# Kernel tuning notes

Measured on AMD Instinct MI355X. Metric: run time of the kernel, lower is better.

Reference implementation:

```python
import jax, jax.numpy as jnp
import numpy as np

NUM_EXPERTS = 8
TOP_K = 2
HIDDEN = 512
INTER = 2048
BALANCE_COEF = 0.01


def setup_inputs() -> dict:
    key = jax.random.key(0)
    ks = jax.random.split(key, 5)
    B, S = 2, 1024
    scale_in = 1.0 / np.sqrt(HIDDEN)
    scale_mid = 1.0 / np.sqrt(INTER)
    return {
        "hidden_states": jax.random.normal(ks[0], (B, S, HIDDEN), jnp.float32),
        "w_router": jax.random.normal(ks[1], (HIDDEN, NUM_EXPERTS), jnp.float32) * scale_in,
        "b_router": jnp.zeros((NUM_EXPERTS,), jnp.float32),
        "w1": jax.random.normal(ks[2], (NUM_EXPERTS, HIDDEN, INTER), jnp.float32) * scale_in,
        "b1": jnp.zeros((NUM_EXPERTS, INTER), jnp.float32),
        "w2": jax.random.normal(ks[3], (NUM_EXPERTS, INTER, HIDDEN), jnp.float32) * scale_mid,
        "b2": jnp.zeros((NUM_EXPERTS, HIDDEN), jnp.float32),
    }


def reference(hidden_states, w_router, b_router, w1, b1, w2, b2):
    B, S, H = hidden_states.shape
    E, K = NUM_EXPERTS, TOP_K

    # ---- Router: softmax over experts, top-k selection, renormalized weights ----
    logits = jnp.einsum("bsh,he->bse", hidden_states, w_router) + b_router  # (B,S,E)
    probs = jax.nn.softmax(logits, axis=-1)
    top_vals, top_idx = jax.lax.top_k(probs, K)                              # (B,S,K)
    routing_weights = top_vals / jnp.sum(top_vals, axis=-1, keepdims=True)   # renorm to sum 1

    # ---- Load-balancing auxiliary loss: coef * E * sum_e f_e * P_e ----
    assign = jax.nn.one_hot(top_idx, E, dtype=probs.dtype)                   # (B,S,K,E)
    f = jnp.mean(assign, axis=(0, 1, 2))                                     # fraction routed per expert
    P = jnp.mean(probs, axis=(0, 1))                                         # mean router prob per expert
    balance_loss = BALANCE_COEF * E * jnp.sum(f * P)

    # ---- Phase 1: flatten (B,S,H) -> (B*S*K, H) token-slots ----
    T = B * S * K
    tokens_flat = jnp.broadcast_to(hidden_states[:, :, None, :], (B, S, K, H)).reshape(T, H)
    weights_flat = routing_weights.reshape(T)
    experts_flat = top_idx.reshape(T)

    # ---- Phase 2: per-expert MLP, masked combine ----
    out_flat = jnp.zeros_like(tokens_flat)
    for e in range(E):
        hmid = jax.nn.gelu(tokens_flat @ w1[e] + b1[e])                      # (T, INTER)
        y = hmid @ w2[e] + b2[e]                                             # (T, H)
        mask = (experts_flat == e)
        out_flat = out_flat + jnp.where(mask[:, None], y * weights_flat[:, None], 0.0)

    # ---- Phase 3: combine over K and residual ----
    combined = out_flat.reshape(B, S, K, H).sum(axis=2)
    output = combined + hidden_states
    return output, balance_loss
```

## Files before the change

### kernel.cpp

```cpp
#include <hip/hip_runtime.h>
#include <math.h>

#define NT 2048
#define TSLOTS 4096
#define HID 512
#define INTER 2048
#define NE 8
#define TM 128
#define BK 32
#define MAXTILES 40

#define WS_HMID      0
#define WS_PROBS     0
#define WS_TOPIDX    65536
#define WS_TOPW      81920
#define WS_TILE_E    20971520
#define WS_TILE_B    20971776
#define WS_TILE_V    20972032
#define WS_PERM      20972288
#define WS_PW        20992768
#define WS_XB        21013248
#define WS_WT        23110400

typedef __attribute__((ext_vector_type(8))) short bf16x8;
typedef __attribute__((ext_vector_type(4))) float f32x4;
typedef __attribute__((ext_vector_type(8))) unsigned short ushort8;

__device__ __forceinline__ unsigned short f2bf(float f) {
    union { float f; unsigned u; } v; v.f = f;
    unsigned r = v.u + 0x7FFF + ((v.u >> 16) & 1);
    return (unsigned short)(r >> 16);
}

__device__ __forceinline__ void gload16(const void* g, void* l) {
    __builtin_amdgcn_global_load_lds(
        (const __attribute__((address_space(1))) unsigned int*)g,
        (__attribute__((address_space(3))) unsigned int*)l, 16, 0, 0);
}

__device__ __forceinline__ float gelu_tanh(float x) {
    float x3 = x * x * x;
    return 0.5f * x * (1.0f + tanhf(0.7978845608028654f * (x + 0.044715f * x3)));
}

__global__ __launch_bounds__(64) void route_k(
    const float* __restrict__ hs, const float* __restrict__ wr,
    const float* __restrict__ br,
    unsigned short* __restrict__ xb, float* __restrict__ out,
    float* __restrict__ probs, int* __restrict__ topidx, float* __restrict__ topw)
{
    int t = blockIdx.x;
    int lane = threadIdx.x;
    const float* x = hs + (size_t)t * HID + lane * 8;
    float4 v0 = *(const float4*)x;
    float4 v1 = *(const float4*)(x + 4);

    float* o = out + (size_t)t * HID + lane * 8;
    *(float4*)o = v0;
    *(float4*)(o + 4) = v1;

    ushort8 ob;
    ob[0] = f2bf(v0.x); ob[1] = f2bf(v0.y); ob[2] = f2bf(v0.z); ob[3] = f2bf(v0.w);
    ob[4] = f2bf(v1.x); ob[5] = f2bf(v1.y); ob[6] = f2bf(v1.z); ob[7] = f2bf(v1.w);
    *(ushort8*)(xb + (size_t)t * HID + lane * 8) = ob;

    float xv[8] = {v0.x, v0.y, v0.z, v0.w, v1.x, v1.y, v1.z, v1.w};
    float acc[NE];
#pragma unroll
    for (int e = 0; e < NE; e++) acc[e] = 0.0f;
    const float* w = wr + (size_t)lane * 8 * NE;
#pragma unroll
    for (int j = 0; j < 8; j++) {
        float4 wa = *(const float4*)(w + j * NE);
        float4 wb = *(const float4*)(w + j * NE + 4);
        acc[0] += xv[j] * wa.x; acc[1] += xv[j] * wa.y;
        acc[2] += xv[j] * wa.z; acc[3] += xv[j] * wa.w;
        acc[4] += xv[j] * wb.x; acc[5] += xv[j] * wb.y;
        acc[6] += xv[j] * wb.z; acc[7] += xv[j] * wb.w;
    }
#pragma unroll
    for (int off = 32; off > 0; off >>= 1) {
#pragma unroll
        for (int e = 0; e < NE; e++) acc[e] += __shfl_down(acc[e], off);
    }
    if (lane == 0) {
        float l[NE], p[NE];
        float m = -1e30f;
#pragma unroll
        for (int e = 0; e < NE; e++) { l[e] = acc[e] + br[e]; m = fmaxf(m, l[e]); }
        float s = 0.0f;
#pragma unroll
        for (int e = 0; e < NE; e++) { p[e] = expf(l[e] - m); s += p[e]; }
        float inv = 1.0f / s;
#pragma unroll
        for (int e = 0; e < NE; e++) { p[e] *= inv; probs[(size_t)t * NE + e] = p[e]; }
        int i1 = 0;
#pragma unroll
        for (int e = 1; e < NE; e++) if (p[e] > p[i1]) i1 = e;
        int i2 = (i1 == 0) ? 1 : 0;
#pragma unroll
        for (int e = 0; e < NE; e++) if (e != i1 && p[e] > p[i2]) i2 = e;
        float denom = 1.0f / (p[i1] + p[i2]);
        topidx[2 * t]     = i1;
        topidx[2 * t + 1] = i2;
        topw[2 * t]       = p[i1] * denom;
        topw[2 * t + 1]   = p[i2] * denom;
    }
}

__global__ __launch_bounds__(256) void plan_k(
    const float* __restrict__ probs, const int* __restrict__ topidx,
    const float* __restrict__ topw,
    int* __restrict__ tile_e, int* __restrict__ tile_b, int* __restrict__ tile_v,
    int* __restrict__ perm, float* __restrict__ pw, float* __restrict__ loss_out)
{
    int tid = threadIdx.x;
    int lane = tid & 63, wave = tid >> 6;

    float ps[NE];
    int c[NE];
#pragma unroll
    for (int e = 0; e < NE; e++) { ps[e] = 0.0f; c[e] = 0; }
    for (int t = tid; t < NT; t += 256) {
        float4 p0 = *(const float4*)&probs[(size_t)t * NE];
        float4 p1 = *(const float4*)&probs[(size_t)t * NE + 4];
        ps[0] += p0.x; ps[1] += p0.y; ps[2] += p0.z; ps[3] += p0.w;
        ps[4] += p1.x; ps[5] += p1.y; ps[6] += p1.z; ps[7] += p1.w;
    }
    for (int t = tid; t < TSLOTS; t += 256) c[topidx[t]]++;
#pragma unroll
    for (int off = 32; off > 0; off >>= 1) {
#pragma unroll
        for (int e = 0; e < NE; e++) {
            ps[e] += __shfl_down(ps[e], off);
            c[e]  += __shfl_down(c[e], off);
        }
    }
    __shared__ float sps[4][NE];
    __shared__ int sc[4][NE];
    __shared__ int scur[NE];
    if (lane == 0) {
#pragma unroll
        for (int e = 0; e < NE; e++) { sps[wave][e] = ps[e]; sc[wave][e] = c[e]; }
    }
    __syncthreads();
    if (tid == 0) {
        float loss = 0.0f;
        int b = 0, tidx = 0;
        for (int e = 0; e < NE; e++) {
            float pse = sps[0][e] + sps[1][e] + sps[2][e] + sps[3][e];
            int ce = sc[0][e] + sc[1][e] + sc[2][e] + sc[3][e];
            loss += ((float)ce / (float)TSLOTS) * (pse / (float)NT);
            int nt = (ce + TM - 1) / TM;
            scur[e] = b;
            for (int i = 0; i < nt; i++) {
                tile_e[tidx] = e;
                tile_b[tidx] = b + i * TM;
                int v = ce - i * TM;
                tile_v[tidx] = v > TM ? TM : v;
                tidx++;
            }
            b += nt * TM;
        }
        for (; tidx < MAXTILES; tidx++) tile_e[tidx] = -1;
        loss_out[0] = 0.01f * (float)NE * loss;
    }
    __syncthreads();
    for (int t = tid; t < TSLOTS; t += 256) {
        int e = topidx[t];
        int p = atomicAdd(&scur[e], 1);
        perm[p] = t;
        pw[p] = topw[t];
    }
}

__global__ __launch_bounds__(256) void convT_k(const float* __restrict__ src,
                                               unsigned short* __restrict__ dst,
                                               int K, int N)
{
    int e = blockIdx.z;
    int n0 = blockIdx.x * 32, k0 = blockIdx.y * 32;
    const float* s = src + (size_t)e * K * N;
    unsigned short* d = dst + (size_t)e * N * K;
    __shared__ float T[32][33];
    int tid = threadIdx.x;
    int r = tid >> 3, c4 = (tid & 7) * 4;
    float4 v = *(const float4*)(s + (size_t)(k0 + r) * N + n0 + c4);
    T[r][c4 + 0] = v.x; T[r][c4 + 1] = v.y; T[r][c4 + 2] = v.z; T[r][c4 + 3] = v.w;
    __syncthreads();
    ushort4 o;
    o.x = f2bf(T[c4 + 0][r]); o.y = f2bf(T[c4 + 1][r]);
    o.z = f2bf(T[c4 + 2][r]); o.w = f2bf(T[c4 + 3][r]);
    *(ushort4*)(d + (size_t)(n0 + r) * K + k0 + c4) = o;
}

__global__ __launch_bounds__(256) void gemm1_k(
    const unsigned short* __restrict__ xb, const unsigned short* __restrict__ w1t,
    const float* __restrict__ b1,
    const int* __restrict__ tile_e, const int* __restrict__ tile_b,
    const int* __restrict__ tile_v, const int* __restrict__ perm,
    unsigned short* __restrict__ hmid)
{
    int tt = blockIdx.y;
    int e = tile_e[tt];
    if (e < 0) return;
    int p0 = tile_b[tt], nv = tile_v[tt];
    int n0 = blockIdx.x * 128;

    __shared__ unsigned short As[128 * BK];
    __shared__ unsigned short Bs[128 * BK];

    int tid = threadIdx.x;
    int lane = tid & 63, wave = tid >> 6;
    int wm = (wave >> 1) * 64, wn = (wave & 1) * 64;

    int r1 = tid >> 2, r2 = 64 + r1;
    int kseg = (tid & 3) * 8;
    int tok1 = perm[p0 + ((r1 < nv) ? r1 : 0)] >> 1;
    int tok2 = perm[p0 + ((r2 < nv) ? r2 : 0)] >> 1;
    const unsigned short* a1p = xb + (size_t)tok1 * HID + kseg;
    const unsigned short* a2p = xb + (size_t)tok2 * HID + kseg;
    const unsigned short* bbase = w1t + (size_t)e * INTER * HID;
    const unsigned short* b1p = bbase + (size_t)(n0 + r1) * HID + kseg;
    const unsigned short* b2p = bbase + (size_t)(n0 + r2) * HID + kseg;

    f32x4 acc[4][4] = {};
    int fm = lane & 15, fq = lane >> 4;

    for (int k0 = 0; k0 < HID; k0 += BK) {
        __syncthreads();
        gload16(a1p + k0, (void*)(As + tid * 8));
        gload16(a2p + k0, (void*)(As + 2048 + tid * 8));
        gload16(b1p + k0, (void*)(Bs + tid * 8));
        gload16(b2p + k0, (void*)(Bs + 2048 + tid * 8));
        __syncthreads();
        bf16x8 af[4], bfr[4];
#pragma unroll
        for (int t = 0; t < 4; t++)
            af[t] = *(const bf16x8*)&As[(wm + t * 16 + fm) * BK + fq * 8];
#pragma unroll
        for (int t = 0; t < 4; t++)
            bfr[t] = *(const bf16x8*)&Bs[(wn + t * 16 + fm) * BK + fq * 8];
#pragma unroll
        for (int mt = 0; mt < 4; mt++)
#pragma unroll
            for (int nt = 0; nt < 4; nt++)
                acc[mt][nt] = __builtin_amdgcn_mfma_f32_16x16x32_bf16(
                    af[mt], bfr[nt], acc[mt][nt], 0, 0, 0);
    }

    int cn = lane & 15, crb = (lane >> 4) * 4;
#pragma unroll
    for (int mt = 0; mt < 4; mt++) {
#pragma unroll
        for (int r = 0; r < 4; r++) {
            int m = wm + mt * 16 + crb + r;
            size_t rowoff = (size_t)(p0 + m) * INTER;
#pragma unroll
            for (int nt = 0; nt < 4; nt++) {
                int gn = n0 + wn + nt * 16 + cn;
                float vv = acc[mt][nt][r] + b1[e * INTER + gn];
                hmid[rowoff + gn] = f2bf(gelu_tanh(vv));
            }
        }
    }
}

__global__ __launch_bounds__(256) void gemm2_k(
    const unsigned short* __restrict__ hmid, const unsigned short* __restrict__ w2t,
    const float* __restrict__ b2,
    const int* __restrict__ tile_e, const int* __restrict__ tile_b,
    const int* __restrict__ tile_v, const int* __restrict__ perm,
    const float* __restrict__ pw, float* __restrict__ out)
{
    int tt = blockIdx.y;
    int e = tile_e[tt];
    if (e < 0) return;
    int p0 = tile_b[tt], nv = tile_v[tt];
    int n0 = blockIdx.x * 128;
    int kz = blockIdx.z;
    int kbeg = kz * (INTER / 4), kend = kbeg + INTER / 4;

    __shared__ unsigned short As[128 * BK];
    __shared__ unsigned short Bs[128 * BK];

    int tid = threadIdx.x;
    int lane = tid & 63, wave = tid >> 6;
    int wm = (wave >> 1) * 64, wn = (wave & 1) * 64;

    int r1 = tid >> 2, r2 = 64 + r1;
    int kseg = (tid & 3) * 8;
    const unsigned short* a1p = hmid + (size_t)(p0 + r1) * INTER + kseg;
    const unsigned short* a2p = hmid + (size_t)(p0 + r2) * INTER + kseg;
    const unsigned short* bbase = w2t + (size_t)e * HID * INTER;
    const unsigned short* b1p = bbase + (size_t)(n0 + r1) * INTER + kseg;
    const unsigned short* b2p = bbase + (size_t)(n0 + r2) * INTER + kseg;

    f32x4 acc[4][4] = {};
    int fm = lane & 15, fq = lane >> 4;

    for (int k0 = kbeg; k0 < kend; k0 += BK) {
        __syncthreads();
        gload16(a1p + k0, (void*)(As + tid * 8));
        gload16(a2p + k0, (void*)(As + 2048 + tid * 8));
        gload16(b1p + k0, (void*)(Bs + tid * 8));
        gload16(b2p + k0, (void*)(Bs + 2048 + tid * 8));
        __syncthreads();
        bf16x8 af[4], bfr[4];
#pragma unroll
        for (int t = 0; t < 4; t++)
            af[t] = *(const bf16x8*)&As[(wm + t * 16 + fm) * BK + fq * 8];
#pragma unroll
        for (int t = 0; t < 4; t++)
            bfr[t] = *(const bf16x8*)&Bs[(wn + t * 16 + fm) * BK + fq * 8];
#pragma unroll
        for (int mt = 0; mt < 4; mt++)
#pragma unroll
            for (int nt = 0; nt < 4; nt++)
                acc[mt][nt] = __builtin_amdgcn_mfma_f32_16x16x32_bf16(
                    af[mt], bfr[nt], acc[mt][nt], 0, 0, 0);
    }

    int cn = lane & 15, crb = (lane >> 4) * 4;
#pragma unroll
    for (int mt = 0; mt < 4; mt++) {
#pragma unroll
        for (int r = 0; r < 4; r++) {
            int m = wm + mt * 16 + crb + r;
            if (m < nv) {
                int slot = perm[p0 + m];
                int tok = slot >> 1;
                float w = pw[p0 + m];
                float* dst = out + (size_t)tok * HID;
#pragma unroll
                for (int nt = 0; nt < 4; nt++) {
                    int gn = n0 + wn + nt * 16 + cn;
                    float bias = (kz == 0) ? b2[e * HID + gn] : 0.0f;
                    atomicAdd(&dst[gn], w * (acc[mt][nt][r] + bias));
                }
            }
        }
    }
}

extern "C" void kernel_launch(void* const* d_in, const int* in_sizes, int n_in,
                              void* d_out, int out_size, void* d_ws, size_t ws_size,
                              hipStream_t stream) {
    const float* hs = (const float*)d_in[0];
    const float* wr = (const float*)d_in[1];
    const float* br = (const float*)d_in[2];
    const float* w1 = (const float*)d_in[3];
    const float* b1 = (const float*)d_in[4];
    const float* w2 = (const float*)d_in[5];
    const float* b2 = (const float*)d_in[6];
    float* out = (float*)d_out;

    char* ws = (char*)d_ws;
    float* probs           = (float*)(ws + WS_PROBS);
    int*   topidx          = (int*)(ws + WS_TOPIDX);
    float* topw            = (float*)(ws + WS_TOPW);
    int*   tile_e          = (int*)(ws + WS_TILE_E);
    int*   tile_b          = (int*)(ws + WS_TILE_B);
    int*   tile_v          = (int*)(ws + WS_TILE_V);
    int*   perm            = (int*)(ws + WS_PERM);
    float* pw              = (float*)(ws + WS_PW);
    unsigned short* xb     = (unsigned short*)(ws + WS_XB);
    unsigned short* wt     = (unsigned short*)(ws + WS_WT);
    unsigned short* hmid   = (unsigned short*)(ws + WS_HMID);

    route_k<<<NT, 64, 0, stream>>>(hs, wr, br, xb, out, probs, topidx, topw);
    plan_k<<<1, 256, 0, stream>>>(probs, topidx, topw, tile_e, tile_b, tile_v,
                                  perm, pw, out + (size_t)NT * HID);
    convT_k<<<dim3(INTER / 32, HID / 32, NE), 256, 0, stream>>>(w1, wt, HID, INTER);
    gemm1_k<<<dim3(INTER / 128, MAXTILES), 256, 0, stream>>>(
        xb, wt, b1, tile_e, tile_b, tile_v, perm, hmid);
    convT_k<<<dim3(HID / 32, INTER / 32, NE), 256, 0, stream>>>(w2, wt, INTER, HID);
    gemm2_k<<<dim3(HID / 128, MAXTILES, 4), 256, 0, stream>>>(
        hmid, wt, b2, tile_e, tile_b, tile_v, perm, pw, out);
}
```

Baseline: 218.3 us.

## Replace gemm2 atomic scatter with bf16 partial buffers and gather combine kernel

gemm2 no longer scatters weighted results with float atomicAdd into the output. Instead it writes per-slot bf16 partial results for two K-splits into a workspace buffer. A new combine kernel then gathers each token's two slots through an inverse permutation, applies the routing weights and adds the residual. The gemm2 tile also changes to a 128x64 N tile with a 2-way K split instead of 128x128 with a 4-way split. This removes atomic contention and the output pre-initialisation, at the cost of an extra launch, extra workspace traffic, and bf16 rounding of the partial sums.

Measured after the change: 211.7 us. 1.03x faster.

```diff
diff --git a/kernel.cpp b/kernel.cpp
--- a/kernel.cpp
+++ b/kernel.cpp
@@ -9,6 +9,7 @@
 #define TM 128
 #define BK 32
 #define MAXTILES 40
+#define PSLOTS 5120
 
 #define WS_HMID      0
 #define WS_PROBS     0
@@ -19,8 +20,10 @@
 #define WS_TILE_V    20972032
 #define WS_PERM      20972288
 #define WS_PW        20992768
-#define WS_XB        21013248
-#define WS_WT        23110400
+#define WS_ISLOT     21013248
+#define WS_XB        21029632
+#define WS_WT        23126784
+#define WS_Y         39904000
 
 typedef __attribute__((ext_vector_type(8))) short bf16x8;
 typedef __attribute__((ext_vector_type(4))) float f32x4;
@@ -31,6 +34,10 @@
     unsigned r = v.u + 0x7FFF + ((v.u >> 16) & 1);
     return (unsigned short)(r >> 16);
 }
+__device__ __forceinline__ float bf2f(unsigned short b) {
+    union { unsigned u; float f; } v; v.u = ((unsigned)b) << 16;
+    return v.f;
+}
 
 __device__ __forceinline__ void gload16(const void* g, void* l) {
     __builtin_amdgcn_global_load_lds(
@@ -46,7 +53,7 @@
 __global__ __launch_bounds__(64) void route_k(
     const float* __restrict__ hs, const float* __restrict__ wr,
     const float* __restrict__ br,
-    unsigned short* __restrict__ xb, float* __restrict__ out,
+    unsigned short* __restrict__ xb,
     float* __restrict__ probs, int* __restrict__ topidx, float* __restrict__ topw)
 {
     int t = blockIdx.x;
@@ -54,10 +61,6 @@
     const float* x = hs + (size_t)t * HID + lane * 8;
     float4 v0 = *(const float4*)x;
     float4 v1 = *(const float4*)(x + 4);
-
-    float* o = out + (size_t)t * HID + lane * 8;
-    *(float4*)o = v0;
-    *(float4*)(o + 4) = v1;
 
     ushort8 ob;
     ob[0] = f2bf(v0.x); ob[1] = f2bf(v0.y); ob[2] = f2bf(v0.z); ob[3] = f2bf(v0.w);
@@ -112,7 +115,8 @@
     const float* __restrict__ probs, const int* __restrict__ topidx,
     const float* __restrict__ topw,
     int* __restrict__ tile_e, int* __restrict__ tile_b, int* __restrict__ tile_v,
-    int* __restrict__ perm, float* __restrict__ pw, float* __restrict__ loss_out)
+    int* __restrict__ perm, float* __restrict__ pw, int* __restrict__ islot,
+    float* __restrict__ loss_out)
 {
     int tid = threadIdx.x;
     int lane = tid & 63, wave = tid >> 6;
@@ -171,6 +175,7 @@
         int p = atomicAdd(&scur[e], 1);
         perm[p] = t;
         pw[p] = topw[t];
+        islot[t] = p;
     }
 }
 
@@ -270,53 +275,51 @@
     const unsigned short* __restrict__ hmid, const unsigned short* __restrict__ w2t,
     const float* __restrict__ b2,
     const int* __restrict__ tile_e, const int* __restrict__ tile_b,
-    const int* __restrict__ tile_v, const int* __restrict__ perm,
-    const float* __restrict__ pw, float* __restrict__ out)
+    unsigned short* __restrict__ y)
 {
     int tt = blockIdx.y;
     int e = tile_e[tt];
     if (e < 0) return;
-    int p0 = tile_b[tt], nv = tile_v[tt];
-    int n0 = blockIdx.x * 128;
+    int p0 = tile_b[tt];
+    int n0 = blockIdx.x * 64;
     int kz = blockIdx.z;
-    int kbeg = kz * (INTER / 4), kend = kbeg + INTER / 4;
+    int kbeg = kz * (INTER / 2), kend = kbeg + INTER / 2;
+    unsigned short* yk = y + (size_t)kz * PSLOTS * HID;
 
     __shared__ unsigned short As[128 * BK];
-    __shared__ unsigned short Bs[128 * BK];
+    __shared__ unsigned short Bs[64 * BK];
 
     int tid = threadIdx.x;
     int lane = tid & 63, wave = tid >> 6;
-    int wm = (wave >> 1) * 64, wn = (wave & 1) * 64;
+    int wm = (wave >> 1) * 64, wn = (wave & 1) * 32;
 
     int r1 = tid >> 2, r2 = 64 + r1;
     int kseg = (tid & 3) * 8;
     const unsigned short* a1p = hmid + (size_t)(p0 + r1) * INTER + kseg;
     const unsigned short* a2p = hmid + (size_t)(p0 + r2) * INTER + kseg;
     const unsigned short* bbase = w2t + (size_t)e * HID * INTER;
-    const unsigned short* b1p = bbase + (size_t)(n0 + r1) * INTER + kseg;
-    const unsigned short* b2p = bbase + (size_t)(n0 + r2) * INTER + kseg;
-
-    f32x4 acc[4][4] = {};
+    const unsigned short* bp = bbase + (size_t)(n0 + r1) * INTER + kseg;
+
+    f32x4 acc[4][2] = {};
     int fm = lane & 15, fq = lane >> 4;
 
     for (int k0 = kbeg; k0 < kend; k0 += BK) {
         __syncthreads();
         gload16(a1p + k0, (void*)(As + tid * 8));
         gload16(a2p + k0, (void*)(As + 2048 + tid * 8));
-        gload16(b1p + k0, (void*)(Bs + tid * 8));
-        gload16(b2p + k0, (void*)(Bs + 2048 + tid * 8));
+        gload16(bp + k0, (void*)(Bs + tid * 8));
         __syncthreads();
-        bf16x8 af[4], bfr[4];
+        bf16x8 af[4], bfr[2];
 #pragma unroll
         for (int t = 0; t < 4; t++)
             af[t] = *(const bf16x8*)&As[(wm + t * 16 + fm) * BK + fq * 8];
 #pragma unroll
-        for (int t = 0; t < 4; t++)
+        for (int t = 0; t < 2; t++)
             bfr[t] = *(const bf16x8*)&Bs[(wn + t * 16 + fm) * BK + fq * 8];
 #pragma unroll
         for (int mt = 0; mt < 4; mt++)
 #pragma unroll
-            for (int nt = 0; nt < 4; nt++)
+            for (int nt = 0; nt < 2; nt++)
                 acc[mt][nt] = __builtin_amdgcn_mfma_f32_16x16x32_bf16(
                     af[mt], bfr[nt], acc[mt][nt], 0, 0, 0);
     }
@@ -327,20 +330,47 @@
 #pragma unroll
         for (int r = 0; r < 4; r++) {
             int m = wm + mt * 16 + crb + r;
-            if (m < nv) {
-                int slot = perm[p0 + m];
-                int tok = slot >> 1;
-                float w = pw[p0 + m];
-                float* dst = out + (size_t)tok * HID;
-#pragma unroll
-                for (int nt = 0; nt < 4; nt++) {
-                    int gn = n0 + wn + nt * 16 + cn;
-                    float bias = (kz == 0) ? b2[e * HID + gn] : 0.0f;
-                    atomicAdd(&dst[gn], w * (acc[mt][nt][r] + bias));
-                }
+            size_t rowoff = (size_t)(p0 + m) * HID;
+#pragma unroll
+            for (int nt = 0; nt < 2; nt++) {
+                int gn = n0 + wn + nt * 16 + cn;
+                float bias = (kz == 0) ? b2[e * HID + gn] : 0.0f;
+                yk[rowoff + gn] = f2bf(acc[mt][nt][r] + bias);
             }
         }
     }
+}
+
+__global__ __launch_bounds__(64) void combine_k(
+    const float* __restrict__ hs, const unsigned short* __restrict__ y,
+    const int* __restrict__ islot, const float* __restrict__ pw,
+    float* __restrict__ out)
+{
+    int t = blockIdx.x;
+    int lane = threadIdx.x;
+    int pA = islot[2 * t], pB = islot[2 * t + 1];
+    float wA = pw[pA], wB = pw[pB];
+    int c = lane * 8;
+    const unsigned short* yA0 = y + (size_t)pA * HID + c;
+    const unsigned short* yB0 = y + (size_t)pB * HID + c;
+    const unsigned short* yA1 = yA0 + (size_t)PSLOTS * HID;
+    const unsigned short* yB1 = yB0 + (size_t)PSLOTS * HID;
+    ushort8 a0 = *(const ushort8*)yA0;
+    ushort8 a1 = *(const ushort8*)yA1;
+    ushort8 b0 = *(const ushort8*)yB0;
+    ushort8 b1 = *(const ushort8*)yB1;
+    const float* h = hs + (size_t)t * HID + c;
+    float4 h0 = *(const float4*)h;
+    float4 h1 = *(const float4*)(h + 4);
+    float o[8];
+#pragma unroll
+    for (int j = 0; j < 8; j++)
+        o[j] = wA * (bf2f(a0[j]) + bf2f(a1[j])) + wB * (bf2f(b0[j]) + bf2f(b1[j]));
+    float4 r0 = {o[0] + h0.x, o[1] + h0.y, o[2] + h0.z, o[3] + h0.w};
+    float4 r1 = {o[4] + h1.x, o[5] + h1.y, o[6] + h1.z, o[7] + h1.w};
+    float* op = out + (size_t)t * HID + c;
+    *(float4*)op = r0;
+    *(float4*)(op + 4) = r1;
 }
 
 extern "C" void kernel_launch(void* const* d_in, const int* in_sizes, int n_in,
@@ -364,17 +394,20 @@
     int*   tile_v          = (int*)(ws + WS_TILE_V);
     int*   perm            = (int*)(ws + WS_PERM);
     float* pw              = (float*)(ws + WS_PW);
+    int*   islot           = (int*)(ws + WS_ISLOT);
     unsigned short* xb     = (unsigned short*)(ws + WS_XB);
     unsigned short* wt     = (unsigned short*)(ws + WS_WT);
     unsigned short* hmid   = (unsigned short*)(ws + WS_HMID);
-
-    route_k<<<NT, 64, 0, stream>>>(hs, wr, br, xb, out, probs, topidx, topw);
+    unsigned short* y      = (unsigned short*)(ws + WS_Y);
+
+    route_k<<<NT, 64, 0, stream>>>(hs, wr, br, xb, probs, topidx, topw);
     plan_k<<<1, 256, 0, stream>>>(probs, topidx, topw, tile_e, tile_b, tile_v,
-                                  perm, pw, out + (size_t)NT * HID);
+                                  perm, pw, islot, out + (size_t)NT * HID);
     convT_k<<<dim3(INTER / 32, HID / 32, NE), 256, 0, stream>>>(w1, wt, HID, INTER);
     gemm1_k<<<dim3(INTER / 128, MAXTILES), 256, 0, stream>>>(
         xb, wt, b1, tile_e, tile_b, tile_v, perm, hmid);
     convT_k<<<dim3(HID / 32, INTER / 32, NE), 256, 0, stream>>>(w2, wt, INTER, HID);
-    gemm2_k<<<dim3(HID / 128, MAXTILES, 4), 256, 0, stream>>>(
-        hmid, wt, b2, tile_e, tile_b, tile_v, perm, pw, out);
-}
+    gemm2_k<<<dim3(HID / 64, MAXTILES, 2), 256, 0, stream>>>(
+        hmid, wt, b2, tile_e, tile_b, y);
+    combine_k<<<NT, 64, 0, stream>>>(hs, y, islot, pw, out);
+}
```
